# Performance work log

Hardware: AMD Instinct MI355X
Metric: run time of the kernel (lower is better)

The kernel has to match this reference:

```python
import jax, jax.numpy as jnp
import numpy as np

N_HEAD = 16
EPS = 1e-5


def setup_inputs() -> dict:
    key = jax.random.key(0)
    ks = jax.random.split(key, 9)
    B, T, C = 2, 1024, 1024
    s = 0.02
    return {
        "x": jax.random.normal(ks[0], (B, T, C), jnp.float32),
        "Wq": jax.random.normal(ks[1], (C, C), jnp.float32) * s,
        "Wk": jax.random.normal(ks[2], (C, C), jnp.float32) * s,
        "Wv": jax.random.normal(ks[3], (C, C), jnp.float32) * s,
        "Wq2": jax.random.normal(ks[4], (C, C), jnp.float32) * s,
        "Wk2": jax.random.normal(ks[5], (C, C), jnp.float32) * s,
        "Wo": jax.random.normal(ks[6], (C, C), jnp.float32) * s,
        "mixture": jnp.full((1,), -5.0, jnp.float32),  # quartet_gate_init
        "quartet_scale": jnp.ones((1,), jnp.float32),
    }


def reference(x, Wq, Wk, Wv, Wq2, Wk2, Wo, mixture, quartet_scale):
    B, T, C = x.shape
    H = N_HEAD
    Dh = C // H
    scale = 1.0 / jnp.sqrt(jnp.asarray(Dh, x.dtype))

    def heads(W):
        # torch Linear: y = x @ W.T ; then view(B,T,H,Dh).transpose(1,2)
        return (x @ W.T).reshape(B, T, H, Dh).transpose(0, 2, 1, 3)  # [B,H,T,Dh]

    q, k, v = heads(Wq), heads(Wk), heads(Wv)
    q2, k2 = heads(Wq2), heads(Wk2)

    qk = jnp.einsum("bhqd,bhkd->bhqk", q, k) * scale      # [B,H,T,T]
    q2k2 = jnp.einsum("bhqd,bhkd->bhqk", q2, k2) * scale  # [B,H,T,T]

    def row_norm(s):
        mu = s.mean(axis=-1, keepdims=True)
        sigma = s.std(axis=-1, keepdims=True, ddof=1)  # torch std is unbiased
        return (s - mu) / (sigma + EPS)

    qk_n = row_norm(qk)
    q2k2_n = row_norm(q2k2)
    m = jax.nn.sigmoid(mixture)  # [1], broadcasts
    scores = (1.0 - m) * qk_n + m * (qk_n * q2k2_n) * quartet_scale

    causal = jnp.tril(jnp.ones((T, T), bool))  # [T,T]
    scores = jnp.where(causal, scores, -jnp.inf)
    attn = jax.nn.softmax(scores, axis=-1)  # [B,H,T,T]

    y = jnp.einsum("bhqk,bhkd->bhqd", attn, v)  # [B,H,T,Dh]
    y = y.transpose(0, 2, 1, 3).reshape(B, T, C)
    return y @ Wo.T
```

## Files before the change

### kernel.cpp

```cpp
#include <hip/hip_runtime.h>
#include <hip/hip_bf16.h>
#include <stdint.h>

#define TS 1024
#define CS 1024
#define NH 16
#define DHEAD 64
#define NBATCH 2
#define EPSV 1e-5f
#define MEG 1048576

typedef __bf16 bf16x8 __attribute__((ext_vector_type(8)));
typedef __bf16 bf16x4 __attribute__((ext_vector_type(4)));
typedef float  f32x4  __attribute__((ext_vector_type(4)));

#define MFMA(a, b, c) __builtin_amdgcn_mfma_f32_16x16x32_bf16((a), (b), (c), 0, 0, 0)

__device__ __forceinline__ float bf2f(ushort u){
  union { uint32_t i; float f; } v; v.i = ((uint32_t)u) << 16; return v.f;
}
__device__ __forceinline__ ushort f2bf(float f){
  union { float f; uint32_t i; } v; v.f = f;
  uint32_t r = v.i + 0x7FFFu + ((v.i >> 16) & 1u);
  return (ushort)(r >> 16);
}

__device__ __forceinline__ void gl_lds16(const ushort* g, ushort* l) {
  __builtin_amdgcn_global_load_lds(
      (const __attribute__((address_space(1))) void*)g,
      (__attribute__((address_space(3))) void*)l, 16, 0, 0);
}

__global__ __launch_bounds__(256)
void cast_all(const float* __restrict__ x,
              const float* __restrict__ Wq, const float* __restrict__ Wk,
              const float* __restrict__ Wv, const float* __restrict__ Wq2,
              const float* __restrict__ Wk2, const float* __restrict__ Wo,
              ushort* __restrict__ xb, ushort* __restrict__ wcat)
{
  const int XC = 524288, TOT = 2097152;
  for (int idx = blockIdx.x * 256 + threadIdx.x; idx < TOT; idx += 524288) {
    const float* s; ushort* d; int c;
    if (idx < XC) { s = x; d = xb; c = idx; }
    else {
      int r = idx - XC; int w = r >> 18; c = r & 262143;
      switch (w) {
        case 0:  s = Wq;  d = wcat;           break;
        case 1:  s = Wk;  d = wcat + 1*MEG;   break;
        case 2:  s = Wv;  d = wcat + 4*MEG;   break;
        case 3:  s = Wq2; d = wcat + 2*MEG;   break;
        case 4:  s = Wk2; d = wcat + 3*MEG;   break;
        default: s = Wo;  d = wcat + 5*MEG;   break;
      }
    }
    float4 v = *(const float4*)(s + (size_t)c * 4);
    ushort4 o; o.x = f2bf(v.x); o.y = f2bf(v.y); o.z = f2bf(v.z); o.w = f2bf(v.w);
    *(ushort4*)(d + (size_t)c * 4) = o;
  }
}

#define BM 128
#define BN 128
#define BKK 32

template<int EPI>
__global__ __launch_bounds__(256, 2)
void gemm_bt(const ushort* __restrict__ A, const ushort* __restrict__ Bt,
             void* __restrict__ Cout,
             int M, int N, int K, int lda, int ldb, int ldc,
             long sA1, long sA2, long sB1, long sB2, long sC1, long sC2,
             float scale)
{
  __shared__ ushort a_s[BM * BKK];
  __shared__ ushort b_s[BN * BKK];

  const int z = blockIdx.z, zh = z >> 4, zl = z & 15;
  A  += (size_t)zh * sA1 + (size_t)zl * sA2;
  Bt += (size_t)zh * sB1 + (size_t)zl * sB2;

  const int n0 = blockIdx.x * BN;
  const int m0 = blockIdx.y * BM;

  const int t  = threadIdx.x;
  const int w  = t >> 6, l = t & 63;
  const int wr = w >> 1, wc = w & 1;
  const int l15 = l & 15, l4 = l >> 4;

  const int rs = l >> 2;
  const int c8 = (l & 3) * 8;

  f32x4 acc[4][4] = {};

  for (int k0 = 0; k0 < K; k0 += BKK) {
    #pragma unroll
    for (int j = 0; j < 2; ++j) {
      int ch = w * 2 + j;
      int r  = ch * 16 + rs;
      gl_lds16(&A [(size_t)(m0 + r) * lda + k0 + c8], &a_s[ch * 512]);
      gl_lds16(&Bt[(size_t)(n0 + r) * ldb + k0 + c8], &b_s[ch * 512]);
    }
    __syncthreads();

    bf16x8 af[4], bfr[4];
    #pragma unroll
    for (int mi = 0; mi < 4; ++mi)
      af[mi] = *(const bf16x8*)&a_s[(wr * 64 + mi * 16 + l15) * BKK + l4 * 8];
    #pragma unroll
    for (int ni = 0; ni < 4; ++ni)
      bfr[ni] = *(const bf16x8*)&b_s[(wc * 64 + ni * 16 + l15) * BKK + l4 * 8];

    #pragma unroll
    for (int mi = 0; mi < 4; ++mi)
      #pragma unroll
      for (int ni = 0; ni < 4; ++ni)
        acc[mi][ni] = MFMA(af[mi], bfr[ni], acc[mi][ni]);

    __syncthreads();
  }

  #pragma unroll
  for (int mi = 0; mi < 4; ++mi) {
    #pragma unroll
    for (int ni = 0; ni < 4; ++ni) {
      int col  = n0 + wc * 64 + ni * 16 + l15;
      int row0 = m0 + wr * 64 + mi * 16 + l4 * 4;
      if (EPI == 0) {
        ushort* C = (ushort*)Cout + (size_t)zh * sC1 + (size_t)zl * sC2;
        #pragma unroll
        for (int e = 0; e < 4; ++e)
          C[(size_t)(row0 + e) * ldc + col] = f2bf(acc[mi][ni][e] * scale);
      } else {
        float* C = (float*)Cout + (size_t)zh * sC1 + (size_t)zl * sC2;
        #pragma unroll
        for (int e = 0; e < 4; ++e)
          C[(size_t)(row0 + e) * ldc + col] = acc[mi][ni][e] * scale;
      }
    }
  }
}

__global__ __launch_bounds__(256, 2)
void gemm_proj(const ushort* __restrict__ A, const ushort* __restrict__ Bt,
               ushort* __restrict__ qb, ushort* __restrict__ kb,
               ushort* __restrict__ q2b, ushort* __restrict__ k2b,
               ushort* __restrict__ vtb,
               ushort* __restrict__ ktb, ushort* __restrict__ k2tb)
{
  __shared__ ushort a_s[BM * BKK];
  __shared__ ushort b_s[BN * BKK];

  const int n0 = blockIdx.x * BN;
  const int m0 = blockIdx.y * BM;

  const int t  = threadIdx.x;
  const int w  = t >> 6, l = t & 63;
  const int wr = w >> 1, wc = w & 1;
  const int l15 = l & 15, l4 = l >> 4;

  const int rs = l >> 2;
  const int c8 = (l & 3) * 8;

  f32x4 acc[4][4] = {};

  for (int k0 = 0; k0 < CS; k0 += BKK) {
    #pragma unroll
    for (int j = 0; j < 2; ++j) {
      int ch = w * 2 + j;
      int r  = ch * 16 + rs;
      gl_lds16(&A [(size_t)(m0 + r) * CS + k0 + c8], &a_s[ch * 512]);
      gl_lds16(&Bt[(size_t)(n0 + r) * CS + k0 + c8], &b_s[ch * 512]);
    }
    __syncthreads();

    bf16x8 af[4], bfr[4];
    #pragma unroll
    for (int mi = 0; mi < 4; ++mi)
      af[mi] = *(const bf16x8*)&a_s[(wr * 64 + mi * 16 + l15) * BKK + l4 * 8];
    #pragma unroll
    for (int ni = 0; ni < 4; ++ni)
      bfr[ni] = *(const bf16x8*)&b_s[(wc * 64 + ni * 16 + l15) * BKK + l4 * 8];

    #pragma unroll
    for (int mi = 0; mi < 4; ++mi)
      #pragma unroll
      for (int ni = 0; ni < 4; ++ni)
        acc[mi][ni] = MFMA(af[mi], bfr[ni], acc[mi][ni]);

    __syncthreads();
  }

  #pragma unroll
  for (int mi = 0; mi < 4; ++mi) {
    #pragma unroll
    for (int ni = 0; ni < 4; ++ni) {
      int col  = n0 + wc * 64 + ni * 16 + l15;
      int row0 = m0 + wr * 64 + mi * 16 + l4 * 4;
      int seg  = col >> 10, cc = col & (CS - 1);
      if (seg < 4) {
        ushort* dst = (seg == 0) ? qb : (seg == 1) ? kb : (seg == 2) ? q2b : k2b;
        float sc = (seg & 1) ? 1.f : 0.125f;
        #pragma unroll
        for (int e = 0; e < 4; ++e)
          dst[(size_t)(row0 + e) * CS + cc] = f2bf(acc[mi][ni][e] * sc);
        if (seg == 1 || seg == 3) {
          int bb = row0 >> 10, tt = row0 & (TS - 1);
          int hh = cc >> 6, dd = cc & (DHEAD - 1);
          ushort* td = (seg == 1) ? ktb : k2tb;
          ushort4 o;
          o.x = f2bf(acc[mi][ni][0]); o.y = f2bf(acc[mi][ni][1]);
          o.z = f2bf(acc[mi][ni][2]); o.w = f2bf(acc[mi][ni][3]);
          *(ushort4*)&td[(((size_t)(bb * NH + hh) * DHEAD + dd) * TS) + tt] = o;
        }
      } else {
        int bb = row0 >> 10, tt = row0 & (TS - 1);
        int hh = cc >> 6, dd = cc & (DHEAD - 1);
        ushort4 o;
        o.x = f2bf(acc[mi][ni][0]); o.y = f2bf(acc[mi][ni][1]);
        o.z = f2bf(acc[mi][ni][2]); o.w = f2bf(acc[mi][ni][3]);
        *(ushort4*)&vtb[(((size_t)(bb * NH + hh) * DHEAD + dd) * TS) + tt] = o;
      }
    }
  }
}

__global__ __launch_bounds__(256, 2)
void gram(const ushort* __restrict__ ktb, const ushort* __restrict__ k2tb,
          ushort* __restrict__ g1b, ushort* __restrict__ g2b,
          float* __restrict__ csb)
{
  __shared__ ushort t_s[64 * 128];

  const int mat = blockIdx.x & 1, z = blockIdx.x >> 1;
  const ushort* S = (mat ? k2tb : ktb) + (size_t)z * DHEAD * TS;

  const int t = threadIdx.x, w = t >> 6, l = t & 63;
  const int l15 = l & 15, l4 = l >> 4;

  f32x4 acc[4] = {};
  float csacc = 0.f;

  for (int tt = 0; tt < 8; ++tt) {
    const int t0 = tt * 128;
    __syncthreads();
    #pragma unroll
    for (int i = 0; i < 4; ++i) {
      int issue = w * 4 + i;
      int row = issue * 4 + l4;
      int gs  = l15 ^ (row & 15);
      gl_lds16(&S[(size_t)row * TS + t0 + gs * 8], &t_s[issue * 512]);
    }
    __syncthreads();

    {
      int r = w * 16 + l15;
      #pragma unroll
      for (int j = 0; j < 4; ++j) {
        int gg = ((l4 * 4 + j) ^ (r & 15)) * 8;
        uint4 vv = *(const uint4*)&t_s[r * 128 + gg];
        const ushort* pu = (const ushort*)&vv;
        #pragma unroll
        for (int e2 = 0; e2 < 8; ++e2) csacc += bf2f(pu[e2]);
      }
    }

    #pragma unroll
    for (int ks = 0; ks < 4; ++ks) {
      int ar = w * 16 + l15;
      bf16x8 af = *(const bf16x8*)&t_s[ar * 128 + ((ks * 4 + l4) ^ (ar & 15)) * 8];
      #pragma unroll
      for (int ni = 0; ni < 4; ++ni) {
        int br = ni * 16 + l15;
        bf16x8 bf_ = *(const bf16x8*)&t_s[br * 128 + ((ks * 4 + l4) ^ (br & 15)) * 8];
        acc[ni] = MFMA(af, bf_, acc[ni]);
      }
    }
  }

  csacc += __shfl_xor(csacc, 16);
  csacc += __shfl_xor(csacc, 32);
  if (l4 == 0)
    csb[(mat * 32 + z) * 64 + w * 16 + l15] = csacc;

  ushort* G = (mat ? g2b : g1b) + (size_t)z * 4096;
  #pragma unroll
  for (int ni = 0; ni < 4; ++ni)
    #pragma unroll
    for (int e = 0; e < 4; ++e)
      G[(w * 16 + l4 * 4 + e) * 64 + ni * 16 + l15] = f2bf(acc[ni][e]);
}

__global__ __launch_bounds__(256, 2)
void attn_fused(const ushort* __restrict__ qb, const ushort* __restrict__ kb,
                const ushort* __restrict__ q2b, const ushort* __restrict__ k2b,
                const ushort* __restrict__ vtb, ushort* __restrict__ yb,
                const ushort* __restrict__ g1b, const ushort* __restrict__ g2b,
                const float* __restrict__ csb,
                const float* __restrict__ mixture, const float* __restrict__ qsc)
{
  __shared__ ushort kbuf [2][4096];
  __shared__ ushort k2buf[2][4096];
  __shared__ ushort vbuf [2][4096];
  __shared__ ushort p_s  [64 * 68];

  const int idx  = blockIdx.x;
  const int xcd  = idx & 7, slot = idx >> 3;
  const int z    = ((slot >> 4) << 3) + xcd;
  const int s4   = slot & 15;
  const int qt   = (s4 & 1) ? (s4 >> 1) : (15 - (s4 >> 1));
  const int b    = z >> 4, h = z & 15;
  const int m0   = qt * 64;

  const ushort* Q  = qb  + (size_t)b * TS * CS + h * DHEAD;
  const ushort* Q2 = q2b + (size_t)b * TS * CS + h * DHEAD;
  const ushort* K  = kb  + (size_t)b * TS * CS + h * DHEAD;
  const ushort* K2 = k2b + (size_t)b * TS * CS + h * DHEAD;
  const ushort* Vt = vtb + (size_t)z * DHEAD * TS;
  const ushort* G1 = g1b + (size_t)z * 4096;
  const ushort* G2 = g2b + (size_t)z * 4096;
  ushort* Y = yb + (size_t)b * TS * CS + h * DHEAD;

  const int t = threadIdx.x, w = t >> 6, l = t & 63;
  const int l15 = l & 15, l4 = l >> 4;
  const int r8 = l >> 3, g7 = l & 7;

  const float gm = 1.f / (1.f + __expf(-mixture[0]));
  const float mq = gm * qsc[0];
  const float om = 1.f - gm;

  auto stage_tile = [&](int ct, int bs) {
    const int t0 = ct * 64;
    #pragma unroll
    for (int i = 0; i < 2; ++i) {
      int issue = w * 2 + i;
      int row = issue * 8 + r8;
      int gs  = g7 ^ (row & 7);
      gl_lds16(&K [(size_t)(t0 + row) * CS + gs * 8], &kbuf [bs][issue * 512]);
      gl_lds16(&K2[(size_t)(t0 + row) * CS + gs * 8], &k2buf[bs][issue * 512]);
      gl_lds16(&Vt[(size_t)row * TS + t0 + gs * 8], &vbuf[bs][issue * 512]);
    }
  };

  #pragma unroll
  for (int i = 0; i < 2; ++i) {
    int issue = w * 2 + i;
    int row = issue * 8 + r8;
    int gs  = g7 ^ (row & 7);
    gl_lds16(&Q [(size_t)(m0 + row) * CS + gs * 8], &kbuf [0][issue * 512]);
    gl_lds16(&Q2[(size_t)(m0 + row) * CS + gs * 8], &k2buf[0][issue * 512]);
    gl_lds16(&G1[row * 64 + gs * 8], &vbuf[0][issue * 512]);
    gl_lds16(&G2[row * 64 + gs * 8], &p_s[issue * 512]);
  }
  stage_tile(0, 1);
  __syncthreads();

  const int qrow = w * 16 + l15;
  bf16x8 fq[2], fq2[2];
  #pragma unroll
  for (int ks = 0; ks < 2; ++ks) {
    int gg = ((ks * 4 + l4) ^ (qrow & 7)) * 8;
    fq [ks] = *(const bf16x8*)&kbuf [0][qrow * 64 + gg];
    fq2[ks] = *(const bf16x8*)&k2buf[0][qrow * 64 + gg];
  }

  f32x4 U1[4] = {}, U2[4] = {};
  #pragma unroll
  for (int ks = 0; ks < 2; ++ks) {
    #pragma unroll
    for (int ni = 0; ni < 4; ++ni) {
      int gr = ni * 16 + l15;
      int gg = ((ks * 4 + l4) ^ (gr & 7)) * 8;
      bf16x8 bg1 = *(const bf16x8*)&vbuf[0][gr * 64 + gg];
      bf16x8 bg2 = *(const bf16x8*)&p_s[gr * 64 + gg];
      U1[ni] = MFMA(fq [ks], bg1, U1[ni]);
      U2[ni] = MFMA(fq2[ks], bg2, U2[ni]);
    }
  }

  float cs1[4], cs2[4];
  #pragma unroll
  for (int ni = 0; ni < 4; ++ni) {
    cs1[ni] = csb[z * 64 + ni * 16 + l15];
    cs2[ni] = csb[2048 + z * 64 + ni * 16 + l15];
  }

  float mu1[4], iv1[4], mu2[4], iv2[4];
  #pragma unroll
  for (int e = 0; e < 4; ++e) {
    int rl = w * 16 + l4 * 4 + e;
    float ssq1 = 0.f, md1 = 0.f, ssq2 = 0.f, md2 = 0.f;
    #pragma unroll
    for (int ni = 0; ni < 4; ++ni) {
      int d  = ni * 16 + l15;
      int ad = rl * 64 + (((d >> 3) ^ (rl & 7)) << 3) + (d & 7);
      float qv1 = bf2f(kbuf [0][ad]);
      float qv2 = bf2f(k2buf[0][ad]);
      ssq1 = fmaf(U1[ni][e], qv1, ssq1); md1 = fmaf(qv1, cs1[ni], md1);
      ssq2 = fmaf(U2[ni][e], qv2, ssq2); md2 = fmaf(qv2, cs2[ni], md2);
    }
    #pragma unroll
    for (int o = 1; o <= 8; o <<= 1) {
      ssq1 += __shfl_xor(ssq1, o); md1 += __shfl_xor(md1, o);
      ssq2 += __shfl_xor(ssq2, o); md2 += __shfl_xor(md2, o);
    }
    float m1 = md1 * (1.f / TS), m2 = md2 * (1.f / TS);
    float v1 = (ssq1 - (float)TS * m1 * m1) * (1.f / (TS - 1));
    float v2 = (ssq2 - (float)TS * m2 * m2) * (1.f / (TS - 1));
    mu1[e] = m1; iv1[e] = 1.f / (sqrtf(fmaxf(v1, 0.f)) + EPSV);
    mu2[e] = m2; iv2[e] = 1.f / (sqrtf(fmaxf(v2, 0.f)) + EPSV);
  }
  __syncthreads();

  float mrow[4], lrow[4];
  #pragma unroll
  for (int e = 0; e < 4; ++e) { mrow[e] = -INFINITY; lrow[e] = 0.f; }
  f32x4 accO[4] = {};

  for (int ct = 0; ct <= qt; ++ct) {
    const int t0  = ct * 64;
    const int cur = (ct & 1) ^ 1;
    if (ct < qt) stage_tile(ct + 1, cur ^ 1);

    const ushort* ks_ = kbuf [cur];
    const ushort* k2s_= k2buf[cur];
    const ushort* vs_ = vbuf [cur];

    f32x4 a1[4] = {}, a2[4] = {};
    #pragma unroll
    for (int ks = 0; ks < 2; ++ks) {
      bf16x8 bk[4], bk2[4];
      #pragma unroll
      for (int ni = 0; ni < 4; ++ni) {
        int j  = ni * 16 + l15;
        int gg = ((ks * 4 + l4) ^ (j & 7)) * 8;
        bk [ni] = *(const bf16x8*)&ks_ [j * 64 + gg];
        bk2[ni] = *(const bf16x8*)&k2s_[j * 64 + gg];
      }
      #pragma unroll
      for (int ni = 0; ni < 4; ++ni) {
        a1[ni] = MFMA(fq [ks], bk [ni], a1[ni]);
        a2[ni] = MFMA(fq2[ks], bk2[ni], a2[ni]);
      }
    }

    float tmax[4];
    #pragma unroll
    for (int e = 0; e < 4; ++e) tmax[e] = -INFINITY;
    #pragma unroll
    for (int ni = 0; ni < 4; ++ni)
      #pragma unroll
      for (int e = 0; e < 4; ++e) {
        int gr = m0 + w * 16 + l4 * 4 + e;
        int gc = t0 + ni * 16 + l15;
        float n1 = (a1[ni][e] - mu1[e]) * iv1[e];
        float n2 = (a2[ni][e] - mu2[e]) * iv2[e];
        float s  = n1 * (om + mq * n2);
        s = (gc <= gr) ? s : -INFINITY;
        a1[ni][e] = s;
        tmax[e] = fmaxf(tmax[e], s);
      }
    #pragma unroll
    for (int o = 1; o <= 8; o <<= 1)
      #pragma unroll
      for (int e = 0; e < 4; ++e)
        tmax[e] = fmaxf(tmax[e], __shfl_xor(tmax[e], o));

    float fac[4];
    #pragma unroll
    for (int e = 0; e < 4; ++e) {
      float mn = fmaxf(mrow[e], tmax[e]);
      fac[e] = __expf(mrow[e] - mn);
      mrow[e] = mn;
      lrow[e] *= fac[e];
    }

    float tsum[4] = {};
    #pragma unroll
    for (int ni = 0; ni < 4; ++ni)
      #pragma unroll
      for (int e = 0; e < 4; ++e) {
        float s = a1[ni][e];
        float p = (s > -INFINITY) ? __expf(s - mrow[e]) : 0.f;
        tsum[e] += p;
        p_s[(w * 16 + l4 * 4 + e) * 68 + ni * 16 + l15] = f2bf(p);
      }
    #pragma unroll
    for (int o = 1; o <= 8; o <<= 1)
      #pragma unroll
      for (int e = 0; e < 4; ++e)
        tsum[e] += __shfl_xor(tsum[e], o);
    #pragma unroll
    for (int e = 0; e < 4; ++e) lrow[e] += tsum[e];
    #pragma unroll
    for (int ni = 0; ni < 4; ++ni)
      #pragma unroll
      for (int e = 0; e < 4; ++e)
        accO[ni][e] *= fac[e];

    #pragma unroll
    for (int ks = 0; ks < 2; ++ks) {
      int po = (w * 16 + l15) * 68 + ks * 32 + l4 * 8;
      bf16x4 plo = *(const bf16x4*)&p_s[po];
      bf16x4 phi = *(const bf16x4*)&p_s[po + 4];
      bf16x8 ap = __builtin_shufflevector(plo, phi, 0, 1, 2, 3, 4, 5, 6, 7);
      bf16x8 bv[4];
      #pragma unroll
      for (int ni = 0; ni < 4; ++ni) {
        int d  = ni * 16 + l15;
        int gg = ((ks * 4 + l4) ^ (d & 7)) * 8;
        bv[ni] = *(const bf16x8*)&vs_[d * 64 + gg];
      }
      #pragma unroll
      for (int ni = 0; ni < 4; ++ni)
        accO[ni] = MFMA(ap, bv[ni], accO[ni]);
    }

    __syncthreads();
  }

  float invl[4];
  #pragma unroll
  for (int e = 0; e < 4; ++e) invl[e] = 1.f / lrow[e];
  #pragma unroll
  for (int ni = 0; ni < 4; ++ni)
    #pragma unroll
    for (int e = 0; e < 4; ++e)
      Y[(size_t)(m0 + w * 16 + l4 * 4 + e) * CS + ni * 16 + l15] =
          f2bf(accO[ni][e] * invl[e]);
}

extern "C" void kernel_launch(void* const* d_in, const int* in_sizes, int n_in,
                              void* d_out, int out_size, void* d_ws, size_t ws_size,
                              hipStream_t stream) {
  const float* x    = (const float*)d_in[0];
  const float* Wq   = (const float*)d_in[1];
  const float* Wk   = (const float*)d_in[2];
  const float* Wv   = (const float*)d_in[3];
  const float* Wq2  = (const float*)d_in[4];
  const float* Wk2  = (const float*)d_in[5];
  const float* Wo   = (const float*)d_in[6];
  const float* mixture = (const float*)d_in[7];
  const float* qsc  = (const float*)d_in[8];
  float* out = (float*)d_out;

  const size_t MT = (size_t)NBATCH * TS;
  ushort* ws = (ushort*)d_ws;
  ushort* xb   = ws;
  ushort* wcat = xb   + (size_t)2 * MEG;
  ushort* qb   = wcat + (size_t)6 * MEG;
  ushort* q2b  = qb   + (size_t)2 * MEG;
  ushort* kb   = q2b  + (size_t)2 * MEG;
  ushort* k2b  = kb   + (size_t)2 * MEG;
  ushort* vtb  = k2b  + (size_t)2 * MEG;
  ushort* yb   = vtb  + (size_t)2 * MEG;
  ushort* ktb  = yb   + (size_t)2 * MEG;
  ushort* k2tb = ktb  + (size_t)2 * MEG;
  ushort* g1b  = k2tb + (size_t)2 * MEG;
  ushort* g2b  = g1b  + (size_t)(MEG / 8);
  float*  csb  = (float*)(g2b + (size_t)(MEG / 8));
  ushort* wob  = wcat + (size_t)5 * MEG;

  cast_all<<<2048, 256, 0, stream>>>(x, Wq, Wk, Wv, Wq2, Wk2, Wo, xb, wcat);

  gemm_proj<<<dim3(5 * CS / BN, MT / BM, 1), 256, 0, stream>>>(
      xb, wcat, qb, kb, q2b, k2b, vtb, ktb, k2tb);

  gram<<<64, 256, 0, stream>>>(ktb, k2tb, g1b, g2b, csb);

  attn_fused<<<512, 256, 0, stream>>>(qb, kb, q2b, k2b, vtb, yb,
                                      g1b, g2b, csb, mixture, qsc);

  gemm_bt<1><<<dim3(CS / BN, MT / BM, 1), 256, 0, stream>>>(
      yb, wob, out, (int)MT, CS, CS, CS, CS, CS, 0, 0, 0, 0, 0, 0, 1.f);
}
```

Before: 121.9 us.

## Transpose score MFMA layout and drop online-softmax max tracking in attention

Swaps MFMA operands so each lane owns one query row. Per-row stats and the softmax sum then reduce across only two shuffle steps instead of per-element 16-lane reductions. Removes the running max and rescaling entirely, relying on the row-normalized scores being bounded, and folds log2e into the mixing constants to use exp2. Applies the causal mask only on the diagonal tile, packs P to bf16 with v_cvt_pk_bf16_f32, and remaps block indices. Skipping the max subtraction risks fp32 overflow if the mixture gate grows large.

Result: faster. 105.1 us (-13.8%).

```diff
diff --git a/kernel.cpp b/kernel.cpp
--- a/kernel.cpp
+++ b/kernel.cpp
@@ -301,12 +301,17 @@
   __shared__ ushort k2buf[2][4096];
   __shared__ ushort vbuf [2][4096];
   __shared__ ushort p_s  [64 * 68];
+  __shared__ float  statf[128];
+  __shared__ float  statl[64];
 
   const int idx  = blockIdx.x;
-  const int xcd  = idx & 7, slot = idx >> 3;
-  const int z    = ((slot >> 4) << 3) + xcd;
-  const int s4   = slot & 15;
-  const int qt   = (s4 & 1) ? (s4 >> 1) : (15 - (s4 >> 1));
+  const int pp   = idx >> 8;
+  const int base = idx & 255;
+  const int xcd  = base & 7;
+  const int mm   = base >> 3;
+  const int qh   = mm & 7;
+  const int z    = (mm >> 3) * 8 + xcd;
+  const int qt   = pp ? qh : (15 - qh);
   const int b    = z >> 4, h = z & 15;
   const int m0   = qt * 64;
 
@@ -322,10 +327,12 @@
   const int t = threadIdx.x, w = t >> 6, l = t & 63;
   const int l15 = l & 15, l4 = l >> 4;
   const int r8 = l >> 3, g7 = l & 7;
-
+  const int qrow = w * 16 + l15;
+
+  const float L2E = 1.44269504f;
   const float gm = 1.f / (1.f + __expf(-mixture[0]));
-  const float mq = gm * qsc[0];
-  const float om = 1.f - gm;
+  const float mq2 = gm * qsc[0] * L2E;
+  const float om2 = (1.f - gm) * L2E;
 
   auto stage_tile = [&](int ct, int bs) {
     const int t0 = ct * 64;
@@ -340,6 +347,8 @@
     }
   };
 
+  if (t < 64)       statf[t]      = csb[z * 64 + t];
+  else if (t < 128) statf[t]      = csb[2048 + z * 64 + (t - 64)];
   #pragma unroll
   for (int i = 0; i < 2; ++i) {
     int issue = w * 2 + i;
@@ -353,7 +362,6 @@
   stage_tile(0, 1);
   __syncthreads();
 
-  const int qrow = w * 16 + l15;
   bf16x8 fq[2], fq2[2];
   #pragma unroll
   for (int ks = 0; ks < 2; ++ks) {
@@ -371,52 +379,45 @@
       int gg = ((ks * 4 + l4) ^ (gr & 7)) * 8;
       bf16x8 bg1 = *(const bf16x8*)&vbuf[0][gr * 64 + gg];
       bf16x8 bg2 = *(const bf16x8*)&p_s[gr * 64 + gg];
-      U1[ni] = MFMA(fq [ks], bg1, U1[ni]);
-      U2[ni] = MFMA(fq2[ks], bg2, U2[ni]);
-    }
-  }
-
-  float cs1[4], cs2[4];
+      U1[ni] = MFMA(bg1, fq [ks], U1[ni]);
+      U2[ni] = MFMA(bg2, fq2[ks], U2[ni]);
+    }
+  }
+
+  float ssq1 = 0.f, md1 = 0.f, ssq2 = 0.f, md2 = 0.f;
   #pragma unroll
   for (int ni = 0; ni < 4; ++ni) {
-    cs1[ni] = csb[z * 64 + ni * 16 + l15];
-    cs2[ni] = csb[2048 + z * 64 + ni * 16 + l15];
-  }
-
-  float mu1[4], iv1[4], mu2[4], iv2[4];
-  #pragma unroll
-  for (int e = 0; e < 4; ++e) {
-    int rl = w * 16 + l4 * 4 + e;
-    float ssq1 = 0.f, md1 = 0.f, ssq2 = 0.f, md2 = 0.f;
-    #pragma unroll
-    for (int ni = 0; ni < 4; ++ni) {
-      int d  = ni * 16 + l15;
-      int ad = rl * 64 + (((d >> 3) ^ (rl & 7)) << 3) + (d & 7);
-      float qv1 = bf2f(kbuf [0][ad]);
-      float qv2 = bf2f(k2buf[0][ad]);
-      ssq1 = fmaf(U1[ni][e], qv1, ssq1); md1 = fmaf(qv1, cs1[ni], md1);
-      ssq2 = fmaf(U2[ni][e], qv2, ssq2); md2 = fmaf(qv2, cs2[ni], md2);
-    }
-    #pragma unroll
-    for (int o = 1; o <= 8; o <<= 1) {
-      ssq1 += __shfl_xor(ssq1, o); md1 += __shfl_xor(md1, o);
-      ssq2 += __shfl_xor(ssq2, o); md2 += __shfl_xor(md2, o);
-    }
-    float m1 = md1 * (1.f / TS), m2 = md2 * (1.f / TS);
-    float v1 = (ssq1 - (float)TS * m1 * m1) * (1.f / (TS - 1));
-    float v2 = (ssq2 - (float)TS * m2 * m2) * (1.f / (TS - 1));
-    mu1[e] = m1; iv1[e] = 1.f / (sqrtf(fmaxf(v1, 0.f)) + EPSV);
-    mu2[e] = m2; iv2[e] = 1.f / (sqrtf(fmaxf(v2, 0.f)) + EPSV);
-  }
+    int gsq = ((ni * 2 + (l4 >> 1)) ^ (qrow & 7));
+    int off = qrow * 64 + gsq * 8 + (l4 & 1) * 4;
+    ushort qa[4], qb2[4];
+    *(uint2*)qa  = *(const uint2*)&kbuf [0][off];
+    *(uint2*)qb2 = *(const uint2*)&k2buf[0][off];
+    float c1[4], c2[4];
+    *(float4*)c1 = *(const float4*)&statf[ni * 16 + l4 * 4];
+    *(float4*)c2 = *(const float4*)&statf[64 + ni * 16 + l4 * 4];
+    #pragma unroll
+    for (int e = 0; e < 4; ++e) {
+      float qv1 = bf2f(qa[e]), qv2 = bf2f(qb2[e]);
+      ssq1 = fmaf(U1[ni][e], qv1, ssq1); md1 = fmaf(qv1, c1[e], md1);
+      ssq2 = fmaf(U2[ni][e], qv2, ssq2); md2 = fmaf(qv2, c2[e], md2);
+    }
+  }
+  ssq1 += __shfl_xor(ssq1, 16); md1 += __shfl_xor(md1, 16);
+  ssq2 += __shfl_xor(ssq2, 16); md2 += __shfl_xor(md2, 16);
+  ssq1 += __shfl_xor(ssq1, 32); md1 += __shfl_xor(md1, 32);
+  ssq2 += __shfl_xor(ssq2, 32); md2 += __shfl_xor(md2, 32);
+
+  const float mu1 = md1 * (1.f / TS), mu2 = md2 * (1.f / TS);
+  const float va1 = (ssq1 - (float)TS * mu1 * mu1) * (1.f / (TS - 1));
+  const float va2 = (ssq2 - (float)TS * mu2 * mu2) * (1.f / (TS - 1));
+  const float iv1 = 1.f / (sqrtf(fmaxf(va1, 0.f)) + EPSV);
+  const float iv2 = 1.f / (sqrtf(fmaxf(va2, 0.f)) + EPSV);
   __syncthreads();
 
-  float mrow[4], lrow[4];
-  #pragma unroll
-  for (int e = 0; e < 4; ++e) { mrow[e] = -INFINITY; lrow[e] = 0.f; }
+  float lrow = 0.f;
   f32x4 accO[4] = {};
 
   for (int ct = 0; ct <= qt; ++ct) {
-    const int t0  = ct * 64;
     const int cur = (ct & 1) ^ 1;
     if (ct < qt) stage_tile(ct + 1, cur ^ 1);
 
@@ -437,68 +438,35 @@
       }
       #pragma unroll
       for (int ni = 0; ni < 4; ++ni) {
-        a1[ni] = MFMA(fq [ks], bk [ni], a1[ni]);
-        a2[ni] = MFMA(fq2[ks], bk2[ni], a2[ni]);
-      }
-    }
-
-    float tmax[4];
-    #pragma unroll
-    for (int e = 0; e < 4; ++e) tmax[e] = -INFINITY;
-    #pragma unroll
-    for (int ni = 0; ni < 4; ++ni)
+        a1[ni] = MFMA(bk [ni], fq [ks], a1[ni]);
+        a2[ni] = MFMA(bk2[ni], fq2[ks], a2[ni]);
+      }
+    }
+
+    const bool diag = (ct == qt);
+    #pragma unroll
+    for (int ni = 0; ni < 4; ++ni) {
+      float pe[4];
       #pragma unroll
       for (int e = 0; e < 4; ++e) {
-        int gr = m0 + w * 16 + l4 * 4 + e;
-        int gc = t0 + ni * 16 + l15;
-        float n1 = (a1[ni][e] - mu1[e]) * iv1[e];
-        float n2 = (a2[ni][e] - mu2[e]) * iv2[e];
-        float s  = n1 * (om + mq * n2);
-        s = (gc <= gr) ? s : -INFINITY;
-        a1[ni][e] = s;
-        tmax[e] = fmaxf(tmax[e], s);
-      }
-    #pragma unroll
-    for (int o = 1; o <= 8; o <<= 1)
-      #pragma unroll
-      for (int e = 0; e < 4; ++e)
-        tmax[e] = fmaxf(tmax[e], __shfl_xor(tmax[e], o));
-
-    float fac[4];
-    #pragma unroll
-    for (int e = 0; e < 4; ++e) {
-      float mn = fmaxf(mrow[e], tmax[e]);
-      fac[e] = __expf(mrow[e] - mn);
-      mrow[e] = mn;
-      lrow[e] *= fac[e];
-    }
-
-    float tsum[4] = {};
-    #pragma unroll
-    for (int ni = 0; ni < 4; ++ni)
-      #pragma unroll
-      for (int e = 0; e < 4; ++e) {
-        float s = a1[ni][e];
-        float p = (s > -INFINITY) ? __expf(s - mrow[e]) : 0.f;
-        tsum[e] += p;
-        p_s[(w * 16 + l4 * 4 + e) * 68 + ni * 16 + l15] = f2bf(p);
-      }
-    #pragma unroll
-    for (int o = 1; o <= 8; o <<= 1)
-      #pragma unroll
-      for (int e = 0; e < 4; ++e)
-        tsum[e] += __shfl_xor(tsum[e], o);
-    #pragma unroll
-    for (int e = 0; e < 4; ++e) lrow[e] += tsum[e];
-    #pragma unroll
-    for (int ni = 0; ni < 4; ++ni)
-      #pragma unroll
-      for (int e = 0; e < 4; ++e)
-        accO[ni][e] *= fac[e];
+        float n1 = (a1[ni][e] - mu1) * iv1;
+        float n2 = (a2[ni][e] - mu2) * iv2;
+        float sc = n1 * fmaf(mq2, n2, om2);
+        float pv = exp2f(sc);
+        if (diag) pv = ((ni * 16 + l4 * 4 + e) <= qrow) ? pv : 0.f;
+        lrow += pv;
+        pe[e] = pv;
+      }
+      uint32_t pk01, pk23;
+      asm("v_cvt_pk_bf16_f32 %0, %1, %2" : "=v"(pk01) : "v"(pe[0]), "v"(pe[1]));
+      asm("v_cvt_pk_bf16_f32 %0, %1, %2" : "=v"(pk23) : "v"(pe[2]), "v"(pe[3]));
+      uint2 pk; pk.x = pk01; pk.y = pk23;
+      *(uint2*)&p_s[qrow * 68 + ni * 16 + l4 * 4] = pk;
+    }
 
     #pragma unroll
     for (int ks = 0; ks < 2; ++ks) {
-      int po = (w * 16 + l15) * 68 + ks * 32 + l4 * 8;
+      int po = qrow * 68 + ks * 32 + l4 * 8;
       bf16x4 plo = *(const bf16x4*)&p_s[po];
       bf16x4 phi = *(const bf16x4*)&p_s[po + 4];
       bf16x8 ap = __builtin_shufflevector(plo, phi, 0, 1, 2, 3, 4, 5, 6, 7);
@@ -517,15 +485,19 @@
     __syncthreads();
   }
 
-  float invl[4];
-  #pragma unroll
-  for (int e = 0; e < 4; ++e) invl[e] = 1.f / lrow[e];
+  lrow += __shfl_xor(lrow, 16);
+  lrow += __shfl_xor(lrow, 32);
+  if (l4 == 0) statl[qrow] = lrow;
+  float il[4];
+  *(float4*)il = *(const float4*)&statl[w * 16 + l4 * 4];
+  #pragma unroll
+  for (int e = 0; e < 4; ++e) il[e] = 1.f / il[e];
   #pragma unroll
   for (int ni = 0; ni < 4; ++ni)
     #pragma unroll
     for (int e = 0; e < 4; ++e)
       Y[(size_t)(m0 + w * 16 + l4 * 4 + e) * CS + ni * 16 + l15] =
-          f2bf(accO[ni][e] * invl[e]);
+          f2bf(accO[ni][e] * il[e]);
 }
 
 extern "C" void kernel_launch(void* const* d_in, const int* in_sizes, int n_in,
```
